# Kernel optimization log

Hardware: AMD Instinct MI355X
Metric: run time of the kernel (lower is better)

Reference implementation:

```python
import jax, jax.numpy as jnp
import numpy as np

N = 50000      # nodes
E = 1600000    # edges per graph
IN = 64
HID = 64
OUT = 64


def _gat_conv(x, edge_index, W, a_src, a_dst, bias):
    """PyG GATConv, heads=1, add_self_loops=True, negative_slope=0.2."""
    n = x.shape[0]
    h = x @ W                                   # [N, d]
    loop = jnp.arange(n, dtype=edge_index.dtype)
    src = jnp.concatenate([edge_index[0], loop])
    dst = jnp.concatenate([edge_index[1], loop])
    e = jax.nn.leaky_relu((h @ a_src)[src] + (h @ a_dst)[dst], negative_slope=0.2)
    m = jax.ops.segment_max(e, dst, num_segments=n)          # stable edge-softmax per dst
    w = jnp.exp(e - m[dst])
    denom = jax.ops.segment_sum(w, dst, num_segments=n)
    alpha = w / denom[dst]                                   # [E+N]
    out = jax.ops.segment_sum(h[src] * alpha[:, None], dst, num_segments=n)
    return out + bias


def setup_inputs() -> dict:
    key = jax.random.key(0)
    ks = jax.random.split(key, 32)

    def glorot(k, shape):
        fan_out = shape[1] if len(shape) > 1 else 1
        lim = (6.0 / (shape[0] + fan_out)) ** 0.5
        return jax.random.uniform(k, shape, minval=-lim, maxval=lim, dtype=jnp.float32)

    inp = {
        "x_ind": jax.random.normal(ks[0], (N, IN), jnp.float32),
        "x_pos": jax.random.normal(ks[1], (N, IN), jnp.float32),
        "edge_ind": jax.random.randint(ks[2], (2, E), 0, N, dtype=jnp.int32),
        "edge_pos": jax.random.randint(ks[3], (2, E), 0, N, dtype=jnp.int32),
        "w1_ind": glorot(ks[4], (IN, HID)),
        "as1_ind": glorot(ks[5], (HID,)),
        "ad1_ind": glorot(ks[6], (HID,)),
        "b1_ind": jnp.zeros((HID,), jnp.float32),
        "w2_ind": glorot(ks[7], (HID, OUT)),
        "as2_ind": glorot(ks[8], (OUT,)),
        "ad2_ind": glorot(ks[9], (OUT,)),
        "b2_ind": jnp.zeros((OUT,), jnp.float32),
        "w1_pos": glorot(ks[10], (IN, HID)),
        "as1_pos": glorot(ks[11], (HID,)),
        "ad1_pos": glorot(ks[12], (HID,)),
        "b1_pos": jnp.zeros((HID,), jnp.float32),
        "w2_pos": glorot(ks[13], (HID, OUT)),
        "as2_pos": glorot(ks[14], (OUT,)),
        "ad2_pos": glorot(ks[15], (OUT,)),
        "b2_pos": jnp.zeros((OUT,), jnp.float32),
        "first_hop_att": glorot(ks[16], (2, HID)),
        "att_weight": glorot(ks[17], (2, OUT)),
        "mlp_w": glorot(ks[18], (OUT, 1)),
        "mlp_b": jnp.zeros((1,), jnp.float32),
    }
    return inp


def reference(x_ind, x_pos, edge_ind, edge_pos,
              w1_ind, as1_ind, ad1_ind, b1_ind,
              w2_ind, as2_ind, ad2_ind, b2_ind,
              w1_pos, as1_pos, ad1_pos, b1_pos,
              w2_pos, as2_pos, ad2_pos, b2_pos,
              first_hop_att, att_weight, mlp_w, mlp_b):
    h_i = jax.nn.relu(_gat_conv(x_ind, edge_ind, w1_ind, as1_ind, ad1_ind, b1_ind))
    h_p = jax.nn.relu(_gat_conv(x_pos, edge_pos, w1_pos, as1_pos, ad1_pos, b1_pos))
    # first-hop branch attention over the two graphs
    s1 = jnp.stack([jnp.sum(first_hop_att[0] * h_i, axis=1),
                    jnp.sum(first_hop_att[1] * h_p, axis=1)], axis=0)  # [2, N]
    a1 = jax.nn.softmax(s1, axis=0)
    fused = a1[0][:, None] * h_i + a1[1][:, None] * h_p
    g_i = _gat_conv(fused, edge_ind, w2_ind, as2_ind, ad2_ind, b2_ind)
    g_p = _gat_conv(fused, edge_pos, w2_pos, as2_pos, ad2_pos, b2_pos)
    s2 = jnp.stack([jnp.sum(att_weight[0] * g_i, axis=1),
                    jnp.sum(att_weight[1] * g_p, axis=1)], axis=0)
    a2 = jax.nn.softmax(s2, axis=0)
    x = a2[0][:, None] * g_i + a2[1][:, None] * g_p
    return x @ mlp_w + mlp_b                    # [N, 1]
```

## Files before the change

kernel.cpp:

```cpp
#include <hip/hip_runtime.h>
#include <hip/hip_fp16.h>

#define ND 64
#define BG 256
#define MAXB 512
#define PCH 16384
#define CAP 9216

__device__ __forceinline__ float lrelu(float x) { return x > 0.f ? x : 0.2f * x; }

__device__ __forceinline__ float wave_sum(float v) {
#pragma unroll
    for (int m = 32; m > 0; m >>= 1) v += __shfl_xor(v, m, 64);
    return v;
}

__device__ __forceinline__ void fma8(float* acc, float w, int4 raw) {
    union { int4 i; __half h[8]; } u;
    u.i = raw;
#pragma unroll
    for (int i = 0; i < 8; i++) acc[i] = fmaf(w, __half2float(u.h[i]), acc[i]);
}


__global__ void init_cursor(int* __restrict__ bcursor, int nb) {
    int t = threadIdx.x;
    if (t < nb) bcursor[t] = t * CAP;
}

__device__ void partition_body(int* hist, int* lcur,
                               const int* __restrict__ eI, const int* __restrict__ eP,
                               int* __restrict__ bcursor, int* __restrict__ part,
                               int N, int E, int nb) {
    int t = threadIdx.x;
    int total = 2 * E;
    int chunkBase = blockIdx.x * PCH;
    int cnt = min(PCH, total - chunkBase);
    if (t < nb) hist[t] = 0;
    __syncthreads();

    if (cnt == PCH) {
        int pk[16];
        unsigned bkp[8];
#pragma unroll
        for (int it = 0; it < 4; it++) {
            int i = t * 4 + it * 4096;
            int e = chunkBase + i;
            int sv[4], dv[4];
            if (e + 3 < E) {
                int4 a = *(const int4*)(eI + e);
                int4 b = *(const int4*)(eI + E + e);
                sv[0] = a.x; sv[1] = a.y; sv[2] = a.z; sv[3] = a.w;
                dv[0] = b.x; dv[1] = b.y; dv[2] = b.z; dv[3] = b.w;
            } else if (e >= E) {
                int4 a = *(const int4*)(eP + (e - E));
                int4 b = *(const int4*)(eP + E + (e - E));
                sv[0] = a.x; sv[1] = a.y; sv[2] = a.z; sv[3] = a.w;
                dv[0] = b.x + N; dv[1] = b.y + N; dv[2] = b.z + N; dv[3] = b.w + N;
            } else {
#pragma unroll
                for (int k = 0; k < 4; k++) {
                    int ee = e + k;
                    if (ee < E) { sv[k] = eI[ee]; dv[k] = eI[E + ee]; }
                    else        { sv[k] = eP[ee - E]; dv[k] = N + eP[E + ee - E]; }
                }
            }
#pragma unroll
            for (int k = 0; k < 4; k++) {
                int j = it * 4 + k;
                int bk = dv[k] >> 8;
                pk[j] = (sv[k] << 8) | (dv[k] & 255);
                atomicAdd(&hist[bk], 1);
                if ((j & 1) == 0) bkp[j >> 1] = (unsigned)bk;
                else bkp[j >> 1] |= (unsigned)bk << 16;
            }
        }
        __syncthreads();
        if (t < nb) lcur[t] = hist[t] ? atomicAdd(&bcursor[t], hist[t]) : 0;
        __syncthreads();
#pragma unroll
        for (int j = 0; j < 16; j++) {
            int bk = (bkp[j >> 1] >> ((j & 1) * 16)) & 0xffff;
            int pos = atomicAdd(&lcur[bk], 1);
            part[pos] = pk[j];
        }
        return;
    }

    int cnt4 = cnt & ~3;
    for (int i = t * 4; i < cnt4; i += 4096) {
        int e = chunkBase + i;
        int4 d; int base;
        if (e + 3 < E)   { d = *(const int4*)(eI + E + e); base = 0; }
        else if (e >= E) { d = *(const int4*)(eP + E + (e - E)); base = N; }
        else {
            int tmp[4];
#pragma unroll
            for (int k = 0; k < 4; k++) {
                int ee = e + k;
                tmp[k] = (ee < E) ? eI[E + ee] : N + eP[E + ee - E];
            }
            d = make_int4(tmp[0], tmp[1], tmp[2], tmp[3]); base = 0;
        }
        atomicAdd(&hist[(base + d.x) >> 8], 1);
        atomicAdd(&hist[(base + d.y) >> 8], 1);
        atomicAdd(&hist[(base + d.z) >> 8], 1);
        atomicAdd(&hist[(base + d.w) >> 8], 1);
    }
    for (int i = cnt4 + t; i < cnt; i += 1024) {
        int e = chunkBase + i;
        int idx = (e < E) ? eI[E + e] : N + eP[E + (e - E)];
        atomicAdd(&hist[idx >> 8], 1);
    }
    __syncthreads();
    if (t < nb) lcur[t] = hist[t] ? atomicAdd(&bcursor[t], hist[t]) : 0;
    __syncthreads();
    for (int i = t; i < cnt; i += 1024) {
        int e = chunkBase + i;
        int s, idx;
        if (e < E) { s = eI[e]; idx = eI[E + e]; }
        else       { s = eP[e - E]; idx = N + eP[E + (e - E)]; }
        int pos = atomicAdd(&lcur[idx >> 8], 1);
        part[pos] = (s << 8) | (idx & 255);
    }
}

__device__ void gemm_body(float* xsAll, int gb,
                          const float* __restrict__ xA, const float* __restrict__ xB,
                          const float* __restrict__ WA, const float* __restrict__ WB,
                          const float* __restrict__ asA, const float* __restrict__ adA,
                          const float* __restrict__ asB, const float* __restrict__ adB,
                          __half* __restrict__ h16, float* __restrict__ ssrc,
                          float* __restrict__ sdst, int N) {
    int half = gb & 1;
    int blk = gb >> 1;
    int wave = threadIdx.x >> 6;
    int lane = threadIdx.x & 63;
    const float* x  = half ? xB : xA;
    const float* W  = half ? WB : WA;
    const float* av_ = half ? asB : asA;
    const float* dv_ = half ? adB : adA;
    int nodeBase = (blk * 16 + wave) * 4;
    float* xs = xsAll + wave * (4 * ND);

    if (nodeBase + 3 < N) {
        *(float4*)&xs[lane * 4] = *(const float4*)&x[(size_t)nodeBase * ND + lane * 4];
    } else if (nodeBase < N) {
#pragma unroll
        for (int i = 0; i < 4; i++) {
            int gi = nodeBase * ND + lane * 4 + i;
            xs[lane * 4 + i] = (gi < N * ND) ? x[gi] : 0.f;
        }
    }
    __syncthreads();
    if (nodeBase >= N) return;

    float4 acc = {0.f, 0.f, 0.f, 0.f};
#pragma unroll
    for (int k = 0; k < ND; k++) {
        float wv = W[k * ND + lane];
        acc.x = fmaf(xs[0 * ND + k], wv, acc.x);
        acc.y = fmaf(xs[1 * ND + k], wv, acc.y);
        acc.z = fmaf(xs[2 * ND + k], wv, acc.z);
        acc.w = fmaf(xs[3 * ND + k], wv, acc.w);
    }
    float av = av_[lane], dv = dv_[lane];
    float s1x = wave_sum(acc.x * av), s2x = wave_sum(acc.x * dv);
    float s1y = wave_sum(acc.y * av), s2y = wave_sum(acc.y * dv);
    float s1z = wave_sum(acc.z * av), s2z = wave_sum(acc.z * dv);
    float s1w = wave_sum(acc.w * av), s2w = wave_sum(acc.w * dv);

    int g0 = half * N + nodeBase;
    h16[(size_t)(g0 + 0) * ND + lane] = __float2half(acc.x);
    if (nodeBase + 1 < N) h16[(size_t)(g0 + 1) * ND + lane] = __float2half(acc.y);
    if (nodeBase + 2 < N) h16[(size_t)(g0 + 2) * ND + lane] = __float2half(acc.z);
    if (nodeBase + 3 < N) h16[(size_t)(g0 + 3) * ND + lane] = __float2half(acc.w);
    if (lane == 0) {
        ssrc[g0] = s1x; sdst[g0] = s2x;
        if (nodeBase + 1 < N) { ssrc[g0 + 1] = s1y; sdst[g0 + 1] = s2y; }
        if (nodeBase + 2 < N) { ssrc[g0 + 2] = s1z; sdst[g0 + 2] = s2z; }
        if (nodeBase + 3 < N) { ssrc[g0 + 3] = s1w; sdst[g0 + 3] = s2w; }
    }
}

__global__ void __launch_bounds__(1024) part_gemm(
        const int* __restrict__ eI, const int* __restrict__ eP,
        int* __restrict__ bcursor, int* __restrict__ part,
        const float* __restrict__ xA, const float* __restrict__ xB,
        const float* __restrict__ WA, const float* __restrict__ WB,
        const float* __restrict__ asA, const float* __restrict__ adA,
        const float* __restrict__ asB, const float* __restrict__ adB,
        __half* __restrict__ h16, float* __restrict__ ssrc, float* __restrict__ sdst,
        int N, int E, int nb, int partBlocks) {
    __shared__ int smem[16 * 4 * ND];
    if (blockIdx.x < partBlocks) {
        partition_body(smem, smem + MAXB, eI, eP, bcursor, part, N, E, nb);
    } else {
        gemm_body((float*)smem, blockIdx.x - partBlocks,
                  xA, xB, WA, WB, asA, adA, asB, adB, h16, ssrc, sdst, N);
    }
}

__global__ void bucket_build(const int* __restrict__ part, const int* __restrict__ bcursor,
                             int* __restrict__ row, int* __restrict__ deg,
                             int* __restrict__ csr, int n2, int N) {
    __shared__ int lhist[BG * 4];
    __shared__ int lrow[BG * 4];
    int b = blockIdx.x, t = threadIdx.x;
    int start = b * CAP;
    int cnt = bcursor[b] - start;
    int cnt4 = cnt & ~3;
    int q1 = N >> 2, q2 = N >> 1, q3 = q1 + q2;
    auto key = [&](int p) {
        int s = p >> 8;
        int q = (s >= q2) ? 2 : 0;
        q += (s >= (q ? q3 : q1)) ? 1 : 0;
        return ((p & 255) << 2) | q;
    };
    lhist[t] = 0;
    __syncthreads();
    for (int j = t * 4; j < cnt4; j += 4096) {
        int4 p = *(const int4*)(part + start + j);
        atomicAdd(&lhist[key(p.x)], 1);
        atomicAdd(&lhist[key(p.y)], 1);
        atomicAdd(&lhist[key(p.z)], 1);
        atomicAdd(&lhist[key(p.w)], 1);
    }
    for (int j = cnt4 + t; j < cnt; j += 1024) atomicAdd(&lhist[key(part[start + j])], 1);
    __syncthreads();
    int v = lhist[t];
    lrow[t] = v;
    __syncthreads();
    for (int off = 1; off < 1024; off <<= 1) {
        int a = (t >= off) ? lrow[t - off] : 0;
        __syncthreads();
        lrow[t] += a;
        __syncthreads();
    }
    int cur = start + lrow[t] - v;
    if (t < BG) {
        int g = b * BG + t;
        if (g < n2) {
            row[g] = start + lrow[4 * t] - lhist[4 * t];
            deg[g] = lhist[4 * t] + lhist[4 * t + 1] + lhist[4 * t + 2] + lhist[4 * t + 3];
        }
    }
    __syncthreads();
    lhist[t] = cur;
    __syncthreads();
    for (int j = t * 4; j < cnt4; j += 4096) {
        int4 p = *(const int4*)(part + start + j);
        int pos;
        pos = atomicAdd(&lhist[key(p.x)], 1); csr[pos] = p.x >> 8;
        pos = atomicAdd(&lhist[key(p.y)], 1); csr[pos] = p.y >> 8;
        pos = atomicAdd(&lhist[key(p.z)], 1); csr[pos] = p.z >> 8;
        pos = atomicAdd(&lhist[key(p.w)], 1); csr[pos] = p.w >> 8;
    }
    for (int j = cnt4 + t; j < cnt; j += 1024) {
        int p = part[start + j];
        int pos = atomicAdd(&lhist[key(p)], 1);
        csr[pos] = p >> 8;
    }
}

__global__ void gemm2_fused(const float* __restrict__ hbig, const float* __restrict__ fha,
                            const float* __restrict__ WA, const float* __restrict__ WB,
                            const float* __restrict__ asA, const float* __restrict__ adA,
                            const float* __restrict__ asB, const float* __restrict__ adB,
                            __half* __restrict__ h16, float* __restrict__ ssrc,
                            float* __restrict__ sdst, int N) {
    __shared__ float xs[4][4 * ND];
    int half = blockIdx.x & 1;
    int blk = blockIdx.x >> 1;
    int wave = threadIdx.x >> 6;
    int lane = threadIdx.x & 63;
    const float* W  = half ? WB : WA;
    const float* av_ = half ? asB : asA;
    const float* dv_ = half ? adB : adA;
    int nodeBase = (blk * 4 + wave) * 4;
    float* xsw = xs[wave];

    if (nodeBase < N) {
        int nd = nodeBase + (lane >> 4);
        int col = (lane & 15) * 4;
        float4 vi = *(const float4*)&hbig[(size_t)nd * ND + col];
        float4 vp = *(const float4*)&hbig[((size_t)N + nd) * ND + col];
        float4 a0 = *(const float4*)&fha[col];
        float4 a1 = *(const float4*)&fha[ND + col];
        float p0 = vi.x * a0.x + vi.y * a0.y + vi.z * a0.z + vi.w * a0.w;
        float p1 = vp.x * a1.x + vp.y * a1.y + vp.z * a1.z + vp.w * a1.w;
#pragma unroll
        for (int m = 1; m <= 8; m <<= 1) {
            p0 += __shfl_xor(p0, m, 64);
            p1 += __shfl_xor(p1, m, 64);
        }
        float mx = fmaxf(p0, p1);
        float e0 = __expf(p0 - mx), e1 = __expf(p1 - mx);
        float inv = 1.f / (e0 + e1);
        float4 f;
        f.x = (e0 * vi.x + e1 * vp.x) * inv;
        f.y = (e0 * vi.y + e1 * vp.y) * inv;
        f.z = (e0 * vi.z + e1 * vp.z) * inv;
        f.w = (e0 * vi.w + e1 * vp.w) * inv;
        *(float4*)&xsw[lane * 4] = f;
    }
    __syncthreads();
    if (nodeBase >= N) return;

    float4 acc = {0.f, 0.f, 0.f, 0.f};
#pragma unroll
    for (int k = 0; k < ND; k++) {
        float wv = W[k * ND + lane];
        acc.x = fmaf(xsw[0 * ND + k], wv, acc.x);
        acc.y = fmaf(xsw[1 * ND + k], wv, acc.y);
        acc.z = fmaf(xsw[2 * ND + k], wv, acc.z);
        acc.w = fmaf(xsw[3 * ND + k], wv, acc.w);
    }
    float av = av_[lane], dv = dv_[lane];
    float s1x = wave_sum(acc.x * av), s2x = wave_sum(acc.x * dv);
    float s1y = wave_sum(acc.y * av), s2y = wave_sum(acc.y * dv);
    float s1z = wave_sum(acc.z * av), s2z = wave_sum(acc.z * dv);
    float s1w = wave_sum(acc.w * av), s2w = wave_sum(acc.w * dv);

    int g0 = half * N + nodeBase;
    h16[(size_t)(g0 + 0) * ND + lane] = __float2half(acc.x);
    h16[(size_t)(g0 + 1) * ND + lane] = __float2half(acc.y);
    h16[(size_t)(g0 + 2) * ND + lane] = __float2half(acc.z);
    h16[(size_t)(g0 + 3) * ND + lane] = __float2half(acc.w);
    if (lane == 0) {
        ssrc[g0] = s1x; sdst[g0] = s2x;
        ssrc[g0 + 1] = s1y; sdst[g0 + 1] = s2y;
        ssrc[g0 + 2] = s1z; sdst[g0 + 2] = s2z;
        ssrc[g0 + 3] = s1w; sdst[g0 + 3] = s2w;
    }
}

__global__ void aggregate_dual(const int* __restrict__ csr, const int* __restrict__ row,
                               const int* __restrict__ deg, const float* __restrict__ ssrc,
                               const float* __restrict__ sdst, const __half* __restrict__ h16,
                               const float* __restrict__ bA, const float* __restrict__ bB,
                               float* __restrict__ out, int N, int relu) {
    int half = blockIdx.x & 1;
    int wave = threadIdx.x >> 6;
    int lane = threadIdx.x & 63;
    int sub  = lane >> 4;
    int l16  = lane & 15;
    int slot = l16 >> 3;
    int fl8  = (l16 & 7) * 8;
    int node = ((blockIdx.x >> 1) * 4 + wave) * 4 + sub;
    bool valid = node < N;
    int g = half * N + node;
    const float* bias = half ? bB : bA;
    const float* ss = ssrc + (size_t)half * N;
    const __half* hh = h16 + (size_t)half * N * ND;

    int start = valid ? row[g] : 0;
    int cnt   = valid ? deg[g] : 0;
    float sd  = valid ? sdst[g] : 0.f;
    float wself = valid ? __expf(lrelu(ss[node] + sd)) : 0.f;

    float acc[8] = {0.f, 0.f, 0.f, 0.f, 0.f, 0.f, 0.f, 0.f};
    float denomp = 0.f;
    int waveBase = sub << 4;

    int c16 = min(16, cnt);
    int sj = (l16 < c16) ? csr[start + l16] : 0;
    float wj = (l16 < c16) ? __expf(lrelu(ss[sj] + sd)) : 0.f;

    for (int base = 0; base < cnt; base += 16) {
        int nb2 = base + 16;
        int sjn = 0; float svn = 0.f; int c16n = cnt - nb2;
        if (nb2 < cnt) {
            sjn = (l16 < c16n) ? csr[start + nb2 + l16] : 0;
            svn = (l16 < c16n) ? ss[sjn] : 0.f;
        }
        denomp += wj;
        int nq = (min(16, cnt - base) + 1) >> 1;
        float w0 = __shfl(wj, waveBase + slot, 64);
        int s0 = __shfl(sj, waveBase + slot, 64);
        int4 r0 = *(const int4*)(hh + (size_t)s0 * ND + fl8);
        if (nq > 1) {
            float w1 = __shfl(wj, waveBase + 2 + slot, 64);
            int s1 = __shfl(sj, waveBase + 2 + slot, 64);
            int4 r1 = *(const int4*)(hh + (size_t)s1 * ND + fl8);
            for (int c = 2; c < nq; c++) {
                float w2 = __shfl(wj, waveBase + c * 2 + slot, 64);
                int s2 = __shfl(sj, waveBase + c * 2 + slot, 64);
                int4 r2 = *(const int4*)(hh + (size_t)s2 * ND + fl8);
                fma8(acc, w0, r0);
                w0 = w1; r0 = r1;
                w1 = w2; r1 = r2;
            }
            fma8(acc, w0, r0);
            fma8(acc, w1, r1);
        } else {
            fma8(acc, w0, r0);
        }
        if (nb2 < cnt) {
            wj = (l16 < c16n) ? __expf(lrelu(svn + sd)) : 0.f;
            sj = sjn;
        }
    }

#pragma unroll
    for (int i = 0; i < 8; i++) acc[i] += __shfl_xor(acc[i], 8, 64);
#pragma unroll
    for (int m = 1; m <= 8; m <<= 1) denomp += __shfl_xor(denomp, m, 64);
    float denom = denomp + wself;

    if (!valid || slot != 0) return;
    int4 rawS = *(const int4*)(hh + (size_t)node * ND + fl8);
    union { int4 i; __half h[8]; } us;
    us.i = rawS;
    float v[8];
#pragma unroll
    for (int i = 0; i < 8; i++)
        v[i] = (acc[i] + wself * __half2float(us.h[i])) / denom + bias[fl8 + i];
    if (relu) {
#pragma unroll
        for (int i = 0; i < 8; i++) v[i] = fmaxf(v[i], 0.f);
    }
    *(float4*)&out[(size_t)g * ND + fl8]     = make_float4(v[0], v[1], v[2], v[3]);
    *(float4*)&out[(size_t)g * ND + fl8 + 4] = make_float4(v[4], v[5], v[6], v[7]);
}

__global__ void branch_att_mlp(const float* __restrict__ hbig, const float* __restrict__ att,
                               const float* __restrict__ mlpw, const float* __restrict__ mlpb,
                               float* __restrict__ out, int n) {
    int gid = blockIdx.x * blockDim.x + threadIdx.x;
    int node = gid >> 6, lane = gid & 63;
    if (node >= n) return;
    float vi = hbig[(size_t)node * ND + lane];
    float vp = hbig[((size_t)n + node) * ND + lane];
    float s0 = wave_sum(att[lane] * vi);
    float s1 = wave_sum(att[ND + lane] * vp);
    float m = fmaxf(s0, s1);
    float a0 = __expf(s0 - m), a1 = __expf(s1 - m);
    float xj = (a0 * vi + a1 * vp) / (a0 + a1);
    float o = wave_sum(xj * mlpw[lane]);
    if (lane == 0) out[node] = o + mlpb[0];
}

extern "C" void kernel_launch(void* const* d_in, const int* in_sizes, int n_in,
                              void* d_out, int out_size, void* d_ws, size_t ws_size,
                              hipStream_t stream) {
    const int N = in_sizes[0] / ND;
    const int E = in_sizes[2] / 2;

    const float* x_ind = (const float*)d_in[0];
    const float* x_pos = (const float*)d_in[1];
    const int*   e_ind = (const int*)d_in[2];
    const int*   e_pos = (const int*)d_in[3];
    const float* w1i = (const float*)d_in[4];
    const float* as1i = (const float*)d_in[5];
    const float* ad1i = (const float*)d_in[6];
    const float* b1i = (const float*)d_in[7];
    const float* w2i = (const float*)d_in[8];
    const float* as2i = (const float*)d_in[9];
    const float* ad2i = (const float*)d_in[10];
    const float* b2i = (const float*)d_in[11];
    const float* w1p = (const float*)d_in[12];
    const float* as1p = (const float*)d_in[13];
    const float* ad1p = (const float*)d_in[14];
    const float* b1p = (const float*)d_in[15];
    const float* w2p = (const float*)d_in[16];
    const float* as2p = (const float*)d_in[17];
    const float* ad2p = (const float*)d_in[18];
    const float* b2p = (const float*)d_in[19];
    const float* fha = (const float*)d_in[20];
    const float* attw = (const float*)d_in[21];
    const float* mlpw = (const float*)d_in[22];
    const float* mlpb = (const float*)d_in[23];

    char* ws = (char*)d_ws;
    size_t off = 0;
    auto alloc = [&](size_t elems) { void* p = ws + off; off += elems * 4; return p; };

    const int n2 = 2 * N;
    const int nb = (n2 + BG - 1) / BG;

    __half* h16 = (__half*)alloc((size_t)n2 * ND / 2);
    float* hbig = (float*)alloc((size_t)n2 * ND);
    float* ssrc = (float*)alloc(n2);
    float* sdst = (float*)alloc(n2);
    int* deg    = (int*)alloc(n2);
    int* rowi   = (int*)alloc(n2);
    int* csr    = (int*)alloc((size_t)nb * CAP);
    int* bcursor= (int*)alloc(MAXB);
    int* part   = (int*)hbig;

    const int partBlocks  = (2 * E + PCH - 1) / PCH;
    const int gemm1Blocks = 2 * ((N + 63) / 64);
    const int gemm2Blocks = 2 * ((N + 15) / 16);
    const int aggBlocks   = 2 * ((N + 15) / 16);
    const int nodeBlocks  = (N + 3) / 4;

    init_cursor<<<1, 512, 0, stream>>>(bcursor, nb);
    part_gemm<<<partBlocks + gemm1Blocks, 1024, 0, stream>>>(
        e_ind, e_pos, bcursor, part,
        x_ind, x_pos, w1i, w1p, as1i, ad1i, as1p, ad1p,
        h16, ssrc, sdst, N, E, nb, partBlocks);
    bucket_build<<<nb, 1024, 0, stream>>>(part, bcursor, rowi, deg, csr, n2, N);

    aggregate_dual<<<aggBlocks, 256, 0, stream>>>(csr, rowi, deg, ssrc, sdst, h16,
                                                  b1i, b1p, hbig, N, 1);

    gemm2_fused<<<gemm2Blocks, 256, 0, stream>>>(hbig, fha, w2i, w2p,
                                                 as2i, ad2i, as2p, ad2p,
                                                 h16, ssrc, sdst, N);
    aggregate_dual<<<aggBlocks, 256, 0, stream>>>(csr, rowi, deg, ssrc, sdst, h16,
                                                  b2i, b2p, hbig, N, 0);
    branch_att_mlp<<<nodeBlocks, 256, 0, stream>>>(hbig, attw, mlpw, mlpb,
                                                   (float*)d_out, N);
}
```

Before: 328.9 us.

## Fuse branch attention into aggregation and use wave-level scan in bucket build

The aggregation kernel now handles both graphs for the same 8 nodes in one block and applies the branch-attention softmax (and the final MLP in the second layer) through LDS. This removes the full-precision hbig round trip and the separate branch_att_mlp kernel. The second GEMM now reads a precomputed fused tensor. The bucket-build prefix sum changes from a barrier-heavy Hillis-Steele loop to shuffle-based wave scans. The gather loop now issues 8 loads unconditionally instead of a software-pipelined variable count. That fixed count may waste loads on low-degree nodes, and part gets its own buffer.

```diff
diff --git a/kernel.cpp b/kernel.cpp
--- a/kernel.cpp
+++ b/kernel.cpp
@@ -21,7 +21,6 @@
 #pragma unroll
     for (int i = 0; i < 8; i++) acc[i] = fmaf(w, __half2float(u.h[i]), acc[i]);
 }
-
 
 __global__ void init_cursor(int* __restrict__ bcursor, int nb) {
     int t = threadIdx.x;
@@ -201,12 +200,69 @@
     }
 }
 
+__global__ void gemm_dual(const float* __restrict__ xA, const float* __restrict__ xB,
+                          const float* __restrict__ WA, const float* __restrict__ WB,
+                          const float* __restrict__ asA, const float* __restrict__ adA,
+                          const float* __restrict__ asB, const float* __restrict__ adB,
+                          __half* __restrict__ h16, float* __restrict__ ssrc,
+                          float* __restrict__ sdst, int N) {
+    __shared__ float xs[4][4 * ND];
+    int half = blockIdx.x & 1;
+    int blk = blockIdx.x >> 1;
+    int wave = threadIdx.x >> 6;
+    int lane = threadIdx.x & 63;
+    const float* x  = half ? xB : xA;
+    const float* W  = half ? WB : WA;
+    const float* av_ = half ? asB : asA;
+    const float* dv_ = half ? adB : adA;
+    int nodeBase = (blk * 4 + wave) * 4;
+    float* xsw = xs[wave];
+    if (nodeBase + 3 < N) {
+        *(float4*)&xsw[lane * 4] = *(const float4*)&x[(size_t)nodeBase * ND + lane * 4];
+    } else if (nodeBase < N) {
+#pragma unroll
+        for (int i = 0; i < 4; i++) {
+            int gi = nodeBase * ND + lane * 4 + i;
+            xsw[lane * 4 + i] = (gi < N * ND) ? x[gi] : 0.f;
+        }
+    }
+    __syncthreads();
+    if (nodeBase >= N) return;
+    float4 acc = {0.f, 0.f, 0.f, 0.f};
+#pragma unroll
+    for (int k = 0; k < ND; k++) {
+        float wv = W[k * ND + lane];
+        acc.x = fmaf(xsw[0 * ND + k], wv, acc.x);
+        acc.y = fmaf(xsw[1 * ND + k], wv, acc.y);
+        acc.z = fmaf(xsw[2 * ND + k], wv, acc.z);
+        acc.w = fmaf(xsw[3 * ND + k], wv, acc.w);
+    }
+    float av = av_[lane], dv = dv_[lane];
+    float s1x = wave_sum(acc.x * av), s2x = wave_sum(acc.x * dv);
+    float s1y = wave_sum(acc.y * av), s2y = wave_sum(acc.y * dv);
+    float s1z = wave_sum(acc.z * av), s2z = wave_sum(acc.z * dv);
+    float s1w = wave_sum(acc.w * av), s2w = wave_sum(acc.w * dv);
+    int g0 = half * N + nodeBase;
+    h16[(size_t)(g0 + 0) * ND + lane] = __float2half(acc.x);
+    if (nodeBase + 1 < N) h16[(size_t)(g0 + 1) * ND + lane] = __float2half(acc.y);
+    if (nodeBase + 2 < N) h16[(size_t)(g0 + 2) * ND + lane] = __float2half(acc.z);
+    if (nodeBase + 3 < N) h16[(size_t)(g0 + 3) * ND + lane] = __float2half(acc.w);
+    if (lane == 0) {
+        ssrc[g0] = s1x; sdst[g0] = s2x;
+        if (nodeBase + 1 < N) { ssrc[g0 + 1] = s1y; sdst[g0 + 1] = s2y; }
+        if (nodeBase + 2 < N) { ssrc[g0 + 2] = s1z; sdst[g0 + 2] = s2z; }
+        if (nodeBase + 3 < N) { ssrc[g0 + 3] = s1w; sdst[g0 + 3] = s2w; }
+    }
+}
+
 __global__ void bucket_build(const int* __restrict__ part, const int* __restrict__ bcursor,
                              int* __restrict__ row, int* __restrict__ deg,
                              int* __restrict__ csr, int n2, int N) {
     __shared__ int lhist[BG * 4];
-    __shared__ int lrow[BG * 4];
+    __shared__ int lexc[BG * 4];
+    __shared__ int wsum[16];
     int b = blockIdx.x, t = threadIdx.x;
+    int wave = t >> 6, lane = t & 63;
     int start = b * CAP;
     int cnt = bcursor[b] - start;
     int cnt4 = cnt & ~3;
@@ -229,24 +285,37 @@
     for (int j = cnt4 + t; j < cnt; j += 1024) atomicAdd(&lhist[key(part[start + j])], 1);
     __syncthreads();
     int v = lhist[t];
-    lrow[t] = v;
-    __syncthreads();
-    for (int off = 1; off < 1024; off <<= 1) {
-        int a = (t >= off) ? lrow[t - off] : 0;
-        __syncthreads();
-        lrow[t] += a;
-        __syncthreads();
-    }
-    int cur = start + lrow[t] - v;
+    int inc = v;
+#pragma unroll
+    for (int m = 1; m < 64; m <<= 1) {
+        int u = __shfl_up(inc, m, 64);
+        if (lane >= m) inc += u;
+    }
+    if (lane == 63) wsum[wave] = inc;
+    __syncthreads();
+    if (wave == 0) {
+        int s = (lane < 16) ? wsum[lane] : 0;
+        int si = s;
+#pragma unroll
+        for (int m = 1; m < 16; m <<= 1) {
+            int u = __shfl_up(si, m, 64);
+            if (lane >= m) si += u;
+        }
+        if (lane < 16) wsum[lane] = si - s;
+    }
+    __syncthreads();
+    int excl = inc - v + wsum[wave];
+    lexc[t] = excl;
+    __syncthreads();
     if (t < BG) {
         int g = b * BG + t;
         if (g < n2) {
-            row[g] = start + lrow[4 * t] - lhist[4 * t];
+            row[g] = start + lexc[4 * t];
             deg[g] = lhist[4 * t] + lhist[4 * t + 1] + lhist[4 * t + 2] + lhist[4 * t + 3];
         }
     }
     __syncthreads();
-    lhist[t] = cur;
+    lhist[t] = start + excl;
     __syncthreads();
     for (int j = t * 4; j < cnt4; j += 4096) {
         int4 p = *(const int4*)(part + start + j);
@@ -263,91 +332,23 @@
     }
 }
 
-__global__ void gemm2_fused(const float* __restrict__ hbig, const float* __restrict__ fha,
-                            const float* __restrict__ WA, const float* __restrict__ WB,
-                            const float* __restrict__ asA, const float* __restrict__ adA,
-                            const float* __restrict__ asB, const float* __restrict__ adB,
-                            __half* __restrict__ h16, float* __restrict__ ssrc,
-                            float* __restrict__ sdst, int N) {
-    __shared__ float xs[4][4 * ND];
-    int half = blockIdx.x & 1;
-    int blk = blockIdx.x >> 1;
+__global__ void aggregate_fused(const int* __restrict__ csr, const int* __restrict__ row,
+                                const int* __restrict__ deg, const float* __restrict__ ssrc,
+                                const float* __restrict__ sdst, const __half* __restrict__ h16,
+                                const float* __restrict__ bA, const float* __restrict__ bB,
+                                const float* __restrict__ att, const float* __restrict__ mlpw,
+                                const float* __restrict__ mlpb, float* __restrict__ outp,
+                                int N, int mode) {
+    __shared__ float lds[2][8][ND];
     int wave = threadIdx.x >> 6;
     int lane = threadIdx.x & 63;
-    const float* W  = half ? WB : WA;
-    const float* av_ = half ? asB : asA;
-    const float* dv_ = half ? adB : adA;
-    int nodeBase = (blk * 4 + wave) * 4;
-    float* xsw = xs[wave];
-
-    if (nodeBase < N) {
-        int nd = nodeBase + (lane >> 4);
-        int col = (lane & 15) * 4;
-        float4 vi = *(const float4*)&hbig[(size_t)nd * ND + col];
-        float4 vp = *(const float4*)&hbig[((size_t)N + nd) * ND + col];
-        float4 a0 = *(const float4*)&fha[col];
-        float4 a1 = *(const float4*)&fha[ND + col];
-        float p0 = vi.x * a0.x + vi.y * a0.y + vi.z * a0.z + vi.w * a0.w;
-        float p1 = vp.x * a1.x + vp.y * a1.y + vp.z * a1.z + vp.w * a1.w;
-#pragma unroll
-        for (int m = 1; m <= 8; m <<= 1) {
-            p0 += __shfl_xor(p0, m, 64);
-            p1 += __shfl_xor(p1, m, 64);
-        }
-        float mx = fmaxf(p0, p1);
-        float e0 = __expf(p0 - mx), e1 = __expf(p1 - mx);
-        float inv = 1.f / (e0 + e1);
-        float4 f;
-        f.x = (e0 * vi.x + e1 * vp.x) * inv;
-        f.y = (e0 * vi.y + e1 * vp.y) * inv;
-        f.z = (e0 * vi.z + e1 * vp.z) * inv;
-        f.w = (e0 * vi.w + e1 * vp.w) * inv;
-        *(float4*)&xsw[lane * 4] = f;
-    }
-    __syncthreads();
-    if (nodeBase >= N) return;
-
-    float4 acc = {0.f, 0.f, 0.f, 0.f};
-#pragma unroll
-    for (int k = 0; k < ND; k++) {
-        float wv = W[k * ND + lane];
-        acc.x = fmaf(xsw[0 * ND + k], wv, acc.x);
-        acc.y = fmaf(xsw[1 * ND + k], wv, acc.y);
-        acc.z = fmaf(xsw[2 * ND + k], wv, acc.z);
-        acc.w = fmaf(xsw[3 * ND + k], wv, acc.w);
-    }
-    float av = av_[lane], dv = dv_[lane];
-    float s1x = wave_sum(acc.x * av), s2x = wave_sum(acc.x * dv);
-    float s1y = wave_sum(acc.y * av), s2y = wave_sum(acc.y * dv);
-    float s1z = wave_sum(acc.z * av), s2z = wave_sum(acc.z * dv);
-    float s1w = wave_sum(acc.w * av), s2w = wave_sum(acc.w * dv);
-
-    int g0 = half * N + nodeBase;
-    h16[(size_t)(g0 + 0) * ND + lane] = __float2half(acc.x);
-    h16[(size_t)(g0 + 1) * ND + lane] = __float2half(acc.y);
-    h16[(size_t)(g0 + 2) * ND + lane] = __float2half(acc.z);
-    h16[(size_t)(g0 + 3) * ND + lane] = __float2half(acc.w);
-    if (lane == 0) {
-        ssrc[g0] = s1x; sdst[g0] = s2x;
-        ssrc[g0 + 1] = s1y; sdst[g0 + 1] = s2y;
-        ssrc[g0 + 2] = s1z; sdst[g0 + 2] = s2z;
-        ssrc[g0 + 3] = s1w; sdst[g0 + 3] = s2w;
-    }
-}
-
-__global__ void aggregate_dual(const int* __restrict__ csr, const int* __restrict__ row,
-                               const int* __restrict__ deg, const float* __restrict__ ssrc,
-                               const float* __restrict__ sdst, const __half* __restrict__ h16,
-                               const float* __restrict__ bA, const float* __restrict__ bB,
-                               float* __restrict__ out, int N, int relu) {
-    int half = blockIdx.x & 1;
-    int wave = threadIdx.x >> 6;
-    int lane = threadIdx.x & 63;
+    int half = wave >> 1;
     int sub  = lane >> 4;
     int l16  = lane & 15;
     int slot = l16 >> 3;
     int fl8  = (l16 & 7) * 8;
-    int node = ((blockIdx.x >> 1) * 4 + wave) * 4 + sub;
+    int ln   = (wave & 1) * 4 + sub;
+    int node = blockIdx.x * 8 + ln;
     bool valid = node < N;
     int g = half * N + node;
     const float* bias = half ? bB : bA;
@@ -375,27 +376,18 @@
             svn = (l16 < c16n) ? ss[sjn] : 0.f;
         }
         denomp += wj;
-        int nq = (min(16, cnt - base) + 1) >> 1;
-        float w0 = __shfl(wj, waveBase + slot, 64);
-        int s0 = __shfl(sj, waveBase + slot, 64);
-        int4 r0 = *(const int4*)(hh + (size_t)s0 * ND + fl8);
-        if (nq > 1) {
-            float w1 = __shfl(wj, waveBase + 2 + slot, 64);
-            int s1 = __shfl(sj, waveBase + 2 + slot, 64);
-            int4 r1 = *(const int4*)(hh + (size_t)s1 * ND + fl8);
-            for (int c = 2; c < nq; c++) {
-                float w2 = __shfl(wj, waveBase + c * 2 + slot, 64);
-                int s2 = __shfl(sj, waveBase + c * 2 + slot, 64);
-                int4 r2 = *(const int4*)(hh + (size_t)s2 * ND + fl8);
-                fma8(acc, w0, r0);
-                w0 = w1; r0 = r1;
-                w1 = w2; r1 = r2;
-            }
-            fma8(acc, w0, r0);
-            fma8(acc, w1, r1);
-        } else {
-            fma8(acc, w0, r0);
-        }
+        float w[8]; int s[8];
+#pragma unroll
+        for (int c = 0; c < 8; c++) {
+            w[c] = __shfl(wj, waveBase + 2 * c + slot, 64);
+            s[c] = __shfl(sj, waveBase + 2 * c + slot, 64);
+        }
+        int4 r[8];
+#pragma unroll
+        for (int c = 0; c < 8; c++)
+            r[c] = *(const int4*)(hh + (size_t)s[c] * ND + fl8);
+#pragma unroll
+        for (int c = 0; c < 8; c++) fma8(acc, w[c], r[c]);
         if (nb2 < cnt) {
             wj = (l16 < c16n) ? __expf(lrelu(svn + sd)) : 0.f;
             sj = sjn;
@@ -408,37 +400,49 @@
     for (int m = 1; m <= 8; m <<= 1) denomp += __shfl_xor(denomp, m, 64);
     float denom = denomp + wself;
 
-    if (!valid || slot != 0) return;
-    int4 rawS = *(const int4*)(hh + (size_t)node * ND + fl8);
-    union { int4 i; __half h[8]; } us;
-    us.i = rawS;
-    float v[8];
-#pragma unroll
-    for (int i = 0; i < 8; i++)
-        v[i] = (acc[i] + wself * __half2float(us.h[i])) / denom + bias[fl8 + i];
-    if (relu) {
-#pragma unroll
-        for (int i = 0; i < 8; i++) v[i] = fmaxf(v[i], 0.f);
-    }
-    *(float4*)&out[(size_t)g * ND + fl8]     = make_float4(v[0], v[1], v[2], v[3]);
-    *(float4*)&out[(size_t)g * ND + fl8 + 4] = make_float4(v[4], v[5], v[6], v[7]);
-}
-
-__global__ void branch_att_mlp(const float* __restrict__ hbig, const float* __restrict__ att,
-                               const float* __restrict__ mlpw, const float* __restrict__ mlpb,
-                               float* __restrict__ out, int n) {
-    int gid = blockIdx.x * blockDim.x + threadIdx.x;
-    int node = gid >> 6, lane = gid & 63;
-    if (node >= n) return;
-    float vi = hbig[(size_t)node * ND + lane];
-    float vp = hbig[((size_t)n + node) * ND + lane];
-    float s0 = wave_sum(att[lane] * vi);
-    float s1 = wave_sum(att[ND + lane] * vp);
-    float m = fmaxf(s0, s1);
-    float a0 = __expf(s0 - m), a1 = __expf(s1 - m);
-    float xj = (a0 * vi + a1 * vp) / (a0 + a1);
-    float o = wave_sum(xj * mlpw[lane]);
-    if (lane == 0) out[node] = o + mlpb[0];
+    if (valid && slot == 0) {
+        int4 rawS = *(const int4*)(hh + (size_t)node * ND + fl8);
+        union { int4 i; __half h[8]; } us;
+        us.i = rawS;
+        float v[8];
+#pragma unroll
+        for (int i = 0; i < 8; i++)
+            v[i] = (acc[i] + wself * __half2float(us.h[i])) / denom + bias[fl8 + i];
+        if (mode == 1) {
+#pragma unroll
+            for (int i = 0; i < 8; i++) v[i] = fmaxf(v[i], 0.f);
+        }
+        *(float4*)&lds[half][ln][fl8]     = make_float4(v[0], v[1], v[2], v[3]);
+        *(float4*)&lds[half][ln][fl8 + 4] = make_float4(v[4], v[5], v[6], v[7]);
+    }
+    __syncthreads();
+
+    int bn = wave * 2 + (lane >> 5);
+    int node2 = blockIdx.x * 8 + bn;
+    if (node2 >= N) return;
+    int c = (lane & 31) * 2;
+    float2 hi = *(float2*)&lds[0][bn][c];
+    float2 hp = *(float2*)&lds[1][bn][c];
+    float p0 = att[c] * hi.x + att[c + 1] * hi.y;
+    float p1 = att[ND + c] * hp.x + att[ND + c + 1] * hp.y;
+#pragma unroll
+    for (int m = 1; m <= 16; m <<= 1) {
+        p0 += __shfl_xor(p0, m, 64);
+        p1 += __shfl_xor(p1, m, 64);
+    }
+    float mx = fmaxf(p0, p1);
+    float e0 = __expf(p0 - mx), e1 = __expf(p1 - mx);
+    float inv = 1.f / (e0 + e1);
+    float fx = (e0 * hi.x + e1 * hp.x) * inv;
+    float fy = (e0 * hi.y + e1 * hp.y) * inv;
+    if (mode == 1) {
+        *(float2*)&outp[(size_t)node2 * ND + c] = make_float2(fx, fy);
+    } else {
+        float o = mlpw[c] * fx + mlpw[c + 1] * fy;
+#pragma unroll
+        for (int m = 1; m <= 16; m <<= 1) o += __shfl_xor(o, m, 64);
+        if ((lane & 31) == 0) outp[node2] = o + mlpb[0];
+    }
 }
 
 extern "C" void kernel_launch(void* const* d_in, const int* in_sizes, int n_in,
@@ -480,20 +484,19 @@
     const int nb = (n2 + BG - 1) / BG;
 
     __half* h16 = (__half*)alloc((size_t)n2 * ND / 2);
-    float* hbig = (float*)alloc((size_t)n2 * ND);
+    float* fused = (float*)alloc((size_t)N * ND);
     float* ssrc = (float*)alloc(n2);
     float* sdst = (float*)alloc(n2);
     int* deg    = (int*)alloc(n2);
     int* rowi   = (int*)alloc(n2);
     int* csr    = (int*)alloc((size_t)nb * CAP);
+    int* part   = (int*)alloc((size_t)nb * CAP);
     int* bcursor= (int*)alloc(MAXB);
-    int* part   = (int*)hbig;
 
     const int partBlocks  = (2 * E + PCH - 1) / PCH;
     const int gemm1Blocks = 2 * ((N + 63) / 64);
     const int gemm2Blocks = 2 * ((N + 15) / 16);
-    const int aggBlocks   = 2 * ((N + 15) / 16);
-    const int nodeBlocks  = (N + 3) / 4;
+    const int aggBlocks   = (N + 7) / 8;
 
     init_cursor<<<1, 512, 0, stream>>>(bcursor, nb);
     part_gemm<<<partBlocks + gemm1Blocks, 1024, 0, stream>>>(
@@ -502,14 +505,15 @@
         h16, ssrc, sdst, N, E, nb, partBlocks);
     bucket_build<<<nb, 1024, 0, stream>>>(part, bcursor, rowi, deg, csr, n2, N);
 
-    aggregate_dual<<<aggBlocks, 256, 0, stream>>>(csr, rowi, deg, ssrc, sdst, h16,
-                                                  b1i, b1p, hbig, N, 1);
-
-    gemm2_fused<<<gemm2Blocks, 256, 0, stream>>>(hbig, fha, w2i, w2p,
-                                                 as2i, ad2i, as2p, ad2p,
-                                                 h16, ssrc, sdst, N);
-    aggregate_dual<<<aggBlocks, 256, 0, stream>>>(csr, rowi, deg, ssrc, sdst, h16,
-                                                  b2i, b2p, hbig, N, 0);
-    branch_att_mlp<<<nodeBlocks, 256, 0, stream>>>(hbig, attw, mlpw, mlpb,
-                                                   (float*)d_out, N);
-}
+    aggregate_fused<<<aggBlocks, 256, 0, stream>>>(csr, rowi, deg, ssrc, sdst, h16,
+                                                   b1i, b1p, fha, mlpw, mlpb,
+                                                   fused, N, 1);
+
+    gemm_dual<<<gemm2Blocks, 256, 0, stream>>>(fused, fused, w2i, w2p,
+                                               as2i, ad2i, as2p, ad2p,
+                                               h16, ssrc, sdst, N);
+
+    aggregate_fused<<<aggBlocks, 256, 0, stream>>>(csr, rowi, deg, ssrc, sdst, h16,
+                                                   b2i, b2p, attw, mlpw, mlpb,
+                                                   (float*)d_out, N, 2);
+}
```

Result: no change. 333.0 us (+1.3%).
